# Optimization experiments

Measured on AMD Instinct MI355X. Metric: run time of the kernel, lower is better.

Reference implementation:

```python
import jax, jax.numpy as jnp
import numpy as np

N_NODES = 50000
IN_CH = 128
HID = 32
HEADS = 4
OUT_CH = 40
NEG_SLOPE = 0.2


def _glorot(key, shape):
    fan_in, fan_out = shape[-1], shape[0]
    lim = jnp.sqrt(6.0 / (fan_in + fan_out))
    return jax.random.uniform(key, shape, jnp.float32, -lim, lim)


def setup_inputs() -> dict:
    key = jax.random.key(0)
    ks = jax.random.split(key, 16)
    x = jax.random.normal(ks[0], (N_NODES, IN_CH), jnp.float32)
    edge_index = jax.random.randint(ks[1], (2, 800000), 0, N_NODES, jnp.int64)
    # layer 0: in -> hid, heads, concat
    W0 = _glorot(ks[2], (HEADS * HID, IN_CH))
    a_src0 = _glorot(ks[3], (HEADS, HID))
    a_dst0 = _glorot(ks[4], (HEADS, HID))
    b0 = jnp.zeros((HEADS * HID,), jnp.float32)
    # layer 1: hid*heads -> hid, heads, concat
    W1 = _glorot(ks[5], (HEADS * HID, HEADS * HID))
    a_src1 = _glorot(ks[6], (HEADS, HID))
    a_dst1 = _glorot(ks[7], (HEADS, HID))
    b1 = jnp.zeros((HEADS * HID,), jnp.float32)
    # layer 2: hid*heads -> out, 1 head, no concat (mean)
    W2 = _glorot(ks[8], (OUT_CH, HEADS * HID))
    a_src2 = _glorot(ks[9], (1, OUT_CH))
    a_dst2 = _glorot(ks[10], (1, OUT_CH))
    b2 = jnp.zeros((OUT_CH,), jnp.float32)
    return dict(x=x, edge_index=edge_index, W0=W0, a_src0=a_src0, a_dst0=a_dst0, b0=b0,
                W1=W1, a_src1=a_src1, a_dst1=a_dst1, b1=b1,
                W2=W2, a_src2=a_src2, a_dst2=a_dst2, b2=b2)


def _gat_conv(x, src, dst, W, a_src, a_dst, b, concat):
    # PyG GATConv (eval mode, dropout off, negative_slope=0.2)
    N = x.shape[0]
    H, C = a_src.shape
    h = (x @ W.T).reshape(N, H, C)                      # [N,H,C]
    al_s = jnp.sum(h * a_src, axis=-1)                  # [N,H]
    al_d = jnp.sum(h * a_dst, axis=-1)                  # [N,H]
    e = jax.nn.leaky_relu(al_s[src] + al_d[dst], NEG_SLOPE)  # [E,H]
    # segment softmax over destination nodes
    m = jax.ops.segment_max(e, dst, num_segments=N)     # [N,H]
    ex = jnp.exp(e - m[dst])
    den = jax.ops.segment_sum(ex, dst, num_segments=N)  # [N,H]
    alpha = ex / den[dst]                               # [E,H]
    out = jax.ops.segment_sum(h[src] * alpha[:, :, None], dst, num_segments=N)  # [N,H,C]
    out = out.reshape(N, H * C) if concat else out.mean(axis=1)
    return out + b


def reference(x, edge_index, W0, a_src0, a_dst0, b0, W1, a_src1, a_dst1, b1, W2, a_src2, a_dst2, b2):
    N = x.shape[0]
    loops = jnp.arange(N, dtype=edge_index.dtype)
    ei = jnp.concatenate([edge_index, jnp.stack([loops, loops])], axis=1)  # add self loops (PyG default)
    src, dst = ei[0], ei[1]
    h = _gat_conv(x, src, dst, W0, a_src0, a_dst0, b0, concat=True)
    h = jax.nn.elu(h)
    h = _gat_conv(h, src, dst, W1, a_src1, a_dst1, b1, concat=True)
    h = jax.nn.elu(h)
    h = _gat_conv(h, src, dst, W2, a_src2, a_dst2, b2, concat=False)
    return jax.nn.log_softmax(h, axis=1)
```

## Files before the change

### kernel.cpp

```cpp
#include <hip/hip_runtime.h>
#include <hip/hip_fp16.h>
#include <math.h>

typedef _Float16 f16x8 __attribute__((ext_vector_type(8)));
typedef _Float16 f16x4 __attribute__((ext_vector_type(4)));
typedef float f32x4 __attribute__((ext_vector_type(4)));

__device__ __forceinline__ int f2oi(float f) {
    int i = __float_as_int(f);
    return i >= 0 ? i : (i ^ 0x7FFFFFFF);
}
__device__ __forceinline__ float oi2f(int i) {
    return __int_as_float(i >= 0 ? i : (i ^ 0x7FFFFFFF));
}

template<int MT, int H>
__global__ __launch_bounds__(256) void gemm_mfma(const float* __restrict__ X,
                                                 const float* __restrict__ W,
                                                 const float* __restrict__ a_src,
                                                 const float* __restrict__ a_dst,
                                                 __half* __restrict__ Hout, int Mout,
                                                 float* __restrict__ als,
                                                 float* __restrict__ ald,
                                                 int* __restrict__ mint, int N) {
    constexpr int LDSB = (MT * 4096 > 16384) ? MT * 4096 : 16384;
    constexpr int HST = (MT == 8) ? 256 : 128;
    __shared__ char ldsb[LDSB];
    __shared__ int lmax[8];

    int tid = threadIdx.x;
    if (tid < 8) lmax[tid] = (int)0x80000000;

    const int nf4 = 16 * MT * 32;
    for (int idx = tid; idx < nf4; idx += 256) {
        int r = idx >> 5, c = idx & 31;
        float4 w = (r < Mout) ? reinterpret_cast<const float4*>(W)[(size_t)r * 32 + c]
                              : make_float4(0.f, 0.f, 0.f, 0.f);
        f16x4 hv;
        hv[0] = (_Float16)w.x; hv[1] = (_Float16)w.y;
        hv[2] = (_Float16)w.z; hv[3] = (_Float16)w.w;
        int byte = r * 256 + ((c * 8) ^ ((r & 7) << 4));
        *reinterpret_cast<f16x4*>(&ldsb[byte]) = hv;
    }
    __syncthreads();

    int l = tid & 63, wv = tid >> 6;
    int lr = l & 15, lk = l >> 4;
    f32x4 acc[2][MT];
#pragma unroll
    for (int rt = 0; rt < 2; rt++)
#pragma unroll
        for (int c = 0; c < MT; c++) acc[rt][c] = (f32x4){0.f, 0.f, 0.f, 0.f};

    const float* xp[2];
#pragma unroll
    for (int rt = 0; rt < 2; rt++) {
        int rg = blockIdx.x * 128 + rt * 64 + wv * 16 + lr;
        if (rg >= N) rg = N - 1;
        xp[rt] = X + (size_t)rg * 128 + lk * 8;
    }

#pragma unroll
    for (int k0 = 0; k0 < 128; k0 += 32) {
        f16x8 a[2];
#pragma unroll
        for (int rt = 0; rt < 2; rt++) {
            float4 x0 = *reinterpret_cast<const float4*>(xp[rt] + k0);
            float4 x1 = *reinterpret_cast<const float4*>(xp[rt] + k0 + 4);
            a[rt][0] = (_Float16)x0.x; a[rt][1] = (_Float16)x0.y;
            a[rt][2] = (_Float16)x0.z; a[rt][3] = (_Float16)x0.w;
            a[rt][4] = (_Float16)x1.x; a[rt][5] = (_Float16)x1.y;
            a[rt][6] = (_Float16)x1.z; a[rt][7] = (_Float16)x1.w;
        }
#pragma unroll
        for (int c = 0; c < MT; c++) {
            int n = 16 * c + lr;
            int byte = n * 256 + (((k0 + lk * 8) * 2) ^ ((n & 7) << 4));
            f16x8 b = *reinterpret_cast<const f16x8*>(&ldsb[byte]);
            acc[0][c] = __builtin_amdgcn_mfma_f32_16x16x32_f16(a[0], b, acc[0][c], 0, 0, 0);
            acc[1][c] = __builtin_amdgcn_mfma_f32_16x16x32_f16(a[1], b, acc[1][c], 0, 0, 0);
        }
    }
    __syncthreads();

#pragma unroll
    for (int rt = 0; rt < 2; rt++)
#pragma unroll
        for (int c = 0; c < MT; c++)
#pragma unroll
            for (int r = 0; r < 4; r++) {
                int rowl = rt * 64 + wv * 16 + lk * 4 + r;
                int col = 16 * c + lr;
                int byte = rowl * HST + ((col * 2) ^ ((rowl & 7) << 4));
                *reinterpret_cast<__half*>(&ldsb[byte]) = __float2half(acc[rt][c][r]);
            }
    __syncthreads();

    int row = tid >> 1, seg = tid & 1;
    int rowg = blockIdx.x * 128 + row;
    if (rowg < N) {
        const int rowB = Mout * 2;
        int segstart = (MT == 8) ? seg * 128 : seg * 48;
        int nch = (MT == 8) ? 8 : (seg ? 2 : 3);
        float hs[H], hd[H];
#pragma unroll
        for (int h = 0; h < H; h++) { hs[h] = 0.f; hd[h] = 0.f; }
        for (int i = 0; i < nch; i++) {
            int cb = segstart + i * 16;
            f16x8 v = *reinterpret_cast<const f16x8*>(
                &ldsb[row * HST + (cb ^ ((row & 7) << 4))]);
            *reinterpret_cast<f16x8*>((char*)Hout + (size_t)rowg * rowB + cb) = v;
            int hh = (H == 1) ? 0 : (cb >> 6);
            int colb = cb >> 1;
            float ps = 0.f, pd = 0.f;
#pragma unroll
            for (int j = 0; j < 8; j++) {
                float f = (float)v[j];
                ps = fmaf(f, a_src[colb + j], ps);
                pd = fmaf(f, a_dst[colb + j], pd);
            }
            hs[hh] += ps; hd[hh] += pd;
        }
        if (H == 4) {
#pragma unroll
            for (int t = 0; t < 2; t++) {
                int hh = 2 * seg + t;
                als[rowg * 4 + hh] = hs[hh];
                ald[rowg * 4 + hh] = hd[hh];
                atomicMax(&lmax[hh], f2oi(hs[hh]));
                atomicMax(&lmax[4 + hh], f2oi(hd[hh]));
            }
        } else {
            float s = hs[0] + __shfl_xor(hs[0], 1, 64);
            float d = hd[0] + __shfl_xor(hd[0], 1, 64);
            if (seg == 0) {
                als[rowg] = s; ald[rowg] = d;
                atomicMax(&lmax[0], f2oi(s));
                atomicMax(&lmax[4], f2oi(d));
            }
        }
    }
    __syncthreads();
    if (tid < H) atomicMax(&mint[tid], lmax[tid]);
    if (tid >= 8 && tid < 8 + H) atomicMax(&mint[4 + tid - 8], lmax[4 + tid - 8]);
}

__global__ __launch_bounds__(256) void p1_hist(const int* __restrict__ src,
                                               const int* __restrict__ dst,
                                               int E_real, int E_tot, int NB, int NBLK,
                                               int EPB, int* __restrict__ cntmat) {
    __shared__ int hist[1024];
    for (int i = threadIdx.x; i < NB; i += 256) hist[i] = 0;
    __syncthreads();
    int e0 = blockIdx.x * EPB;
    int e1 = min(e0 + EPB, E_tot);
    for (int e = e0 + threadIdx.x; e < e1; e += 256) {
        int d = (e < E_real) ? dst[e] : e - E_real;
        atomicAdd(&hist[d >> 6], 1);
    }
    __syncthreads();
    for (int b = threadIdx.x; b < NB; b += 256)
        cntmat[b * NBLK + blockIdx.x] = hist[b];
}

__global__ __launch_bounds__(256) void p_scancols(int* __restrict__ cntmat,
                                                  int* __restrict__ colTot, int NBLK) {
    __shared__ int sh[256];
    int b = blockIdx.x;
    int t = threadIdx.x;
    if (t < NBLK) sh[t] = cntmat[b * NBLK + t];
    __syncthreads();
    if (t == 0) {
        int run = 0;
        for (int i = 0; i < NBLK; i++) { int v = sh[i]; sh[i] = run; run += v; }
        colTot[b] = run;
    }
    __syncthreads();
    if (t < NBLK) cntmat[b * NBLK + t] = sh[t];
}

__global__ __launch_bounds__(256) void p_scancoarse(const int* __restrict__ colTot,
                                                    int* __restrict__ coarseOff,
                                                    int* __restrict__ offsets,
                                                    int NB, int N, int E_tot) {
    __shared__ int sh[256];
    int t = threadIdx.x, base = t * 4;
    int v0 = 0, v1 = 0, v2 = 0, v3 = 0;
    if (base + 0 < NB) v0 = colTot[base + 0];
    if (base + 1 < NB) v1 = colTot[base + 1];
    if (base + 2 < NB) v2 = colTot[base + 2];
    if (base + 3 < NB) v3 = colTot[base + 3];
    int s = v0 + v1 + v2 + v3;
    sh[t] = s;
    __syncthreads();
    for (int off = 1; off < 256; off <<= 1) {
        int u = (t >= off) ? sh[t - off] : 0;
        __syncthreads();
        sh[t] += u;
        __syncthreads();
    }
    int run = sh[t] - s;
    if (base + 0 < NB) { coarseOff[base + 0] = run; run += v0; }
    if (base + 1 < NB) { coarseOff[base + 1] = run; run += v1; }
    if (base + 2 < NB) { coarseOff[base + 2] = run; run += v2; }
    if (base + 3 < NB) { coarseOff[base + 3] = run; }
    if (t == 255) { coarseOff[NB] = sh[255]; offsets[N] = E_tot; }
}

__global__ __launch_bounds__(256) void p2_scatter(const int* __restrict__ src,
                                                  const int* __restrict__ dst,
                                                  int E_real, int E_tot, int NB, int NBLK,
                                                  int EPB, const int* __restrict__ cntmat,
                                                  const int* __restrict__ coarseOff,
                                                  int2* __restrict__ pairs) {
    __shared__ int cur[1024];
    for (int b = threadIdx.x; b < NB; b += 256)
        cur[b] = coarseOff[b] + cntmat[b * NBLK + blockIdx.x];
    __syncthreads();
    int e0 = blockIdx.x * EPB;
    int e1 = min(e0 + EPB, E_tot);
    for (int e = e0 + threadIdx.x; e < e1; e += 256) {
        int s, d;
        if (e < E_real) { s = src[e]; d = dst[e]; } else { s = d = e - E_real; }
        int pos = atomicAdd(&cur[d >> 6], 1);
        pairs[pos] = make_int2(s, d);
    }
}

__global__ __launch_bounds__(256) void p3_bucket(const int2* __restrict__ pairs,
                                                 const int* __restrict__ coarseOff,
                                                 int NB, int N, int* __restrict__ offsets,
                                                 int* __restrict__ csr_src) {
    __shared__ int lh[64], lc[64];
    int b = blockIdx.x;
    int beg = coarseOff[b], end = coarseOff[b + 1];
    int t = threadIdx.x;
    if (t < 64) lh[t] = 0;
    __syncthreads();
    for (int i = beg + t; i < end; i += 256)
        atomicAdd(&lh[pairs[i].y & 63], 1);
    __syncthreads();
    if (t < 64) {
        int v = lh[t];
        int run = v;
#pragma unroll
        for (int off = 1; off < 64; off <<= 1) {
            int o = __shfl_up(run, off, 64);
            if (t >= off) run += o;
        }
        int ex = run - v;
        lc[t] = ex;
        int node = b * 64 + t;
        if (node < N) offsets[node] = beg + ex;
    }
    __syncthreads();
    for (int i = beg + t; i < end; i += 256) {
        int2 p = pairs[i];
        int pos = atomicAdd(&lc[p.y & 63], 1);
        csr_src[beg + pos] = p.x;
    }
}

__global__ __launch_bounds__(256) void gat_agg128(const int* __restrict__ offsets,
                                                  const int* __restrict__ csr_src,
                                                  const __half* __restrict__ h,
                                                  const float* __restrict__ als,
                                                  const float* __restrict__ ald,
                                                  const int* __restrict__ mint,
                                                  const float* __restrict__ bias,
                                                  float* __restrict__ out, int N) {
    __shared__ float wlds[4][64][4];
    __shared__ int   slds[4][64];
    int wid = threadIdx.x >> 6;
    int lane = threadIdx.x & 63;
    int gwid = (blockIdx.x * 256 + threadIdx.x) >> 6;
    int nWaves = (gridDim.x * 256) >> 6;
    int hh = lane >> 4;
    const __half2* h2 = (const __half2*)h;
    const float4* als4 = (const float4*)als;
    const float4* ald4 = (const float4*)ald;
    float2 bv = ((const float2*)bias)[lane];

    float4 shift;
    {
        float v;
        v = oi2f(mint[0]) + oi2f(mint[4]); shift.x = v > 0.f ? v : 0.2f * v;
        v = oi2f(mint[1]) + oi2f(mint[5]); shift.y = v > 0.f ? v : 0.2f * v;
        v = oi2f(mint[2]) + oi2f(mint[6]); shift.z = v > 0.f ? v : 0.2f * v;
        v = oi2f(mint[3]) + oi2f(mint[7]); shift.w = v > 0.f ? v : 0.2f * v;
    }

    for (int n = gwid; n < N; n += nWaves) {
        int beg = offsets[n], end = offsets[n + 1];
        float4 adn = ald4[n];
        float accx = 0.f, accy = 0.f, den = 0.f;

        for (int c0 = beg; c0 < end; c0 += 64) {
            int e = c0 + lane;
            if (e < end) {
                int s = csr_src[e];
                float4 a4 = als4[s];
                float4 w; float v;
                v = a4.x + adn.x; v = v > 0.f ? v : 0.2f * v; w.x = __expf(v - shift.x);
                v = a4.y + adn.y; v = v > 0.f ? v : 0.2f * v; w.y = __expf(v - shift.y);
                v = a4.z + adn.z; v = v > 0.f ? v : 0.2f * v; w.z = __expf(v - shift.z);
                v = a4.w + adn.w; v = v > 0.f ? v : 0.2f * v; w.w = __expf(v - shift.w);
                *reinterpret_cast<float4*>(&wlds[wid][lane][0]) = w;
                slds[wid][lane] = s;
            }
            int cnt = end - c0; if (cnt > 64) cnt = 64;
            int p = 0;
            for (; p + 4 <= cnt; p += 4) {
                float w0 = wlds[wid][p][hh];     int s0 = slds[wid][p];
                float w1 = wlds[wid][p + 1][hh]; int s1 = slds[wid][p + 1];
                float w2 = wlds[wid][p + 2][hh]; int s2 = slds[wid][p + 2];
                float w3 = wlds[wid][p + 3][hh]; int s3 = slds[wid][p + 3];
                float2 f0 = __half22float2(h2[(size_t)s0 * 64 + lane]);
                float2 f1 = __half22float2(h2[(size_t)s1 * 64 + lane]);
                float2 f2 = __half22float2(h2[(size_t)s2 * 64 + lane]);
                float2 f3 = __half22float2(h2[(size_t)s3 * 64 + lane]);
                den += (w0 + w1) + (w2 + w3);
                accx = fmaf(f0.x, w0, fmaf(f1.x, w1, fmaf(f2.x, w2, fmaf(f3.x, w3, accx))));
                accy = fmaf(f0.y, w0, fmaf(f1.y, w1, fmaf(f2.y, w2, fmaf(f3.y, w3, accy))));
            }
            for (; p < cnt; ++p) {
                float w0 = wlds[wid][p][hh]; int s0 = slds[wid][p];
                float2 f0 = __half22float2(h2[(size_t)s0 * 64 + lane]);
                den += w0;
                accx = fmaf(f0.x, w0, accx);
                accy = fmaf(f0.y, w0, accy);
            }
        }
        float inv = 1.f / den;
        float r0 = accx * inv + bv.x;
        float r1 = accy * inv + bv.y;
        float2 o;
        o.x = r0 > 0.f ? r0 : expm1f(r0);
        o.y = r1 > 0.f ? r1 : expm1f(r1);
        ((float2*)out)[(size_t)n * 64 + lane] = o;
    }
}

__global__ __launch_bounds__(256) void gat_agg40_lsm(const int* __restrict__ offsets,
                                                     const int* __restrict__ csr_src,
                                                     const __half* __restrict__ h,
                                                     const float* __restrict__ als,
                                                     const float* __restrict__ ald,
                                                     const int* __restrict__ mint,
                                                     const float* __restrict__ b2,
                                                     float* __restrict__ out, int N) {
    __shared__ float wlds[4][64];
    __shared__ int   slds[4][64];
    int wid = threadIdx.x >> 6;
    int lane = threadIdx.x & 63;
    int gwid = (blockIdx.x * 256 + threadIdx.x) >> 6;
    int nWaves = (gridDim.x * 256) >> 6;

    float shift;
    {
        float v = oi2f(mint[0]) + oi2f(mint[4]);
        shift = v > 0.f ? v : 0.2f * v;
    }

    for (int n = gwid; n < N; n += nWaves) {
        int beg = offsets[n], end = offsets[n + 1];
        float adn = ald[n];
        float acc = 0.f, den = 0.f;

        for (int c0 = beg; c0 < end; c0 += 64) {
            int e = c0 + lane;
            if (e < end) {
                int s = csr_src[e];
                float v = als[s] + adn; v = v > 0.f ? v : 0.2f * v;
                wlds[wid][lane] = __expf(v - shift);
                slds[wid][lane] = s;
            }
            int cnt = end - c0; if (cnt > 64) cnt = 64;
            int p = 0;
            for (; p + 4 <= cnt; p += 4) {
                float w0 = wlds[wid][p];     int s0 = slds[wid][p];
                float w1 = wlds[wid][p + 1]; int s1 = slds[wid][p + 1];
                float w2 = wlds[wid][p + 2]; int s2 = slds[wid][p + 2];
                float w3 = wlds[wid][p + 3]; int s3 = slds[wid][p + 3];
                float h0 = (lane < 40) ? __half2float(h[(size_t)s0 * 40 + lane]) : 0.f;
                float h1 = (lane < 40) ? __half2float(h[(size_t)s1 * 40 + lane]) : 0.f;
                float h2v = (lane < 40) ? __half2float(h[(size_t)s2 * 40 + lane]) : 0.f;
                float h3 = (lane < 40) ? __half2float(h[(size_t)s3 * 40 + lane]) : 0.f;
                den += (w0 + w1) + (w2 + w3);
                acc = fmaf(h0, w0, fmaf(h1, w1, fmaf(h2v, w2, fmaf(h3, w3, acc))));
            }
            for (; p < cnt; ++p) {
                float w0 = wlds[wid][p]; int s0 = slds[wid][p];
                float h0 = (lane < 40) ? __half2float(h[(size_t)s0 * 40 + lane]) : 0.f;
                den += w0;
                acc = fmaf(h0, w0, acc);
            }
        }
        float val = (lane < 40) ? acc / den + b2[lane] : -INFINITY;
        float mx = val;
#pragma unroll
        for (int off = 32; off >= 1; off >>= 1) mx = fmaxf(mx, __shfl_xor(mx, off, 64));
        float pe = (lane < 40) ? __expf(val - mx) : 0.f;
        float sum = pe;
#pragma unroll
        for (int off = 32; off >= 1; off >>= 1) sum += __shfl_xor(sum, off, 64);
        if (lane < 40) out[n * 40 + lane] = val - mx - logf(sum);
    }
}

extern "C" void kernel_launch(void* const* d_in, const int* in_sizes, int n_in,
                              void* d_out, int out_size, void* d_ws, size_t ws_size,
                              hipStream_t stream) {
    const float* x      = (const float*)d_in[0];
    const int*   ei     = (const int*)d_in[1];
    const float* W0     = (const float*)d_in[2];
    const float* a_src0 = (const float*)d_in[3];
    const float* a_dst0 = (const float*)d_in[4];
    const float* b0     = (const float*)d_in[5];
    const float* W1     = (const float*)d_in[6];
    const float* a_src1 = (const float*)d_in[7];
    const float* a_dst1 = (const float*)d_in[8];
    const float* b1     = (const float*)d_in[9];
    const float* W2     = (const float*)d_in[10];
    const float* a_src2 = (const float*)d_in[11];
    const float* a_dst2 = (const float*)d_in[12];
    const float* b2     = (const float*)d_in[13];

    const int N = in_sizes[0] / 128;
    const int E_real = in_sizes[1] / 2;
    const int E_tot = E_real + N;
    const int* src = ei;
    const int* dst = ei + E_real;

    const int EPB  = 4096;
    const int NBLK = (E_tot + EPB - 1) / EPB;
    const int NB   = (N + 63) >> 6;

    unsigned char* ws = (unsigned char*)d_ws;
    const size_t szH16 = (size_t)N * 128 * sizeof(__half);
    const size_t szAcc = (size_t)N * 128 * sizeof(float);
    size_t off = 0;
    __half* bufH    = (__half*)(ws + off); off += szH16;
    float*  bufAcc  = (float*)(ws + off);  off += szAcc;
    int2*   pairs   = (int2*)(ws + off);   off += (size_t)E_tot * sizeof(int2);
    int*    csr_src = (int*)(ws + off);    off += (size_t)E_tot * sizeof(int);
    float*  als     = (float*)(ws + off);  off += (size_t)N * 4 * sizeof(float);
    float*  ald     = (float*)(ws + off);  off += (size_t)N * 4 * sizeof(float);
    int*    cntmat  = (int*)(ws + off);    off += (size_t)NB * NBLK * sizeof(int);
    int*    colTot  = (int*)(ws + off);    off += (size_t)NB * sizeof(int);
    int*    coarseOff = (int*)(ws + off);  off += (size_t)(NB + 1) * sizeof(int);
    int*    offsets = (int*)(ws + off);    off += (size_t)(N + 1) * sizeof(int);
    int*    mint    = (int*)(ws + off);    off += 24 * sizeof(int);

    const int B = 256;
    const int gRows128 = (N + 127) / 128;
    const int gAgg  = 2048;

    hipMemsetAsync(mint, 0x80, 24 * sizeof(int), stream);
    p1_hist<<<NBLK, B, 0, stream>>>(src, dst, E_real, E_tot, NB, NBLK, EPB, cntmat);
    p_scancols<<<NB, B, 0, stream>>>(cntmat, colTot, NBLK);
    p_scancoarse<<<1, B, 0, stream>>>(colTot, coarseOff, offsets, NB, N, E_tot);
    p2_scatter<<<NBLK, B, 0, stream>>>(src, dst, E_real, E_tot, NB, NBLK, EPB, cntmat, coarseOff, pairs);
    p3_bucket<<<NB, B, 0, stream>>>(pairs, coarseOff, NB, N, offsets, csr_src);

    gemm_mfma<8, 4><<<gRows128, B, 0, stream>>>(x, W0, a_src0, a_dst0, bufH, 128, als, ald, mint, N);
    gat_agg128<<<gAgg, B, 0, stream>>>(offsets, csr_src, bufH, als, ald, mint, b0, bufAcc, N);

    gemm_mfma<8, 4><<<gRows128, B, 0, stream>>>(bufAcc, W1, a_src1, a_dst1, bufH, 128, als, ald, mint + 8, N);
    gat_agg128<<<gAgg, B, 0, stream>>>(offsets, csr_src, bufH, als, ald, mint + 8, b1, bufAcc, N);

    gemm_mfma<3, 1><<<gRows128, B, 0, stream>>>(bufAcc, W2, a_src2, a_dst2, bufH, 40, als, ald, mint + 16, N);
    gat_agg40_lsm<<<gAgg, B, 0, stream>>>(offsets, csr_src, bufH, als, ald, mint + 16, b2,
                                          (float*)d_out, N);
}
```

Before: 238.1 us.

## Split edge attention weights into separate precompute kernels before aggregation

Moves the per-edge leaky-relu/exp attention weight computation out of the aggregation kernels into dedicated edge_w4/edge_w1 kernels that write weights to a workspace buffer aliased with the pairs array. The aggregation kernels then read weights and sources directly from global memory in 8-wide unrolled batches, with no LDS staging or wave-level chunking. This is meant to remove LDS round trips and improve memory-level parallelism in the gather loop. In exchange it adds three launches and an extra write and read of the per-edge weight array (16 bytes per edge for the four-head layers).

```diff
diff --git a/kernel.cpp b/kernel.cpp
--- a/kernel.cpp
+++ b/kernel.cpp
@@ -261,26 +261,17 @@
     }
 }
 
-__global__ __launch_bounds__(256) void gat_agg128(const int* __restrict__ offsets,
-                                                  const int* __restrict__ csr_src,
-                                                  const __half* __restrict__ h,
-                                                  const float* __restrict__ als,
-                                                  const float* __restrict__ ald,
-                                                  const int* __restrict__ mint,
-                                                  const float* __restrict__ bias,
-                                                  float* __restrict__ out, int N) {
-    __shared__ float wlds[4][64][4];
-    __shared__ int   slds[4][64];
-    int wid = threadIdx.x >> 6;
+__global__ __launch_bounds__(256) void edge_w4(const int* __restrict__ offsets,
+                                               const int* __restrict__ csr_src,
+                                               const float* __restrict__ als,
+                                               const float* __restrict__ ald,
+                                               const int* __restrict__ mint,
+                                               float4* __restrict__ wexp, int N) {
     int lane = threadIdx.x & 63;
     int gwid = (blockIdx.x * 256 + threadIdx.x) >> 6;
     int nWaves = (gridDim.x * 256) >> 6;
-    int hh = lane >> 4;
-    const __half2* h2 = (const __half2*)h;
     const float4* als4 = (const float4*)als;
     const float4* ald4 = (const float4*)ald;
-    float2 bv = ((const float2*)bias)[lane];
-
     float4 shift;
     {
         float v;
@@ -289,47 +280,86 @@
         v = oi2f(mint[2]) + oi2f(mint[6]); shift.z = v > 0.f ? v : 0.2f * v;
         v = oi2f(mint[3]) + oi2f(mint[7]); shift.w = v > 0.f ? v : 0.2f * v;
     }
-
     for (int n = gwid; n < N; n += nWaves) {
         int beg = offsets[n], end = offsets[n + 1];
         float4 adn = ald4[n];
+        for (int e = beg + lane; e < end; e += 64) {
+            int s = csr_src[e];
+            float4 a4 = als4[s];
+            float4 w; float v;
+            v = a4.x + adn.x; v = v > 0.f ? v : 0.2f * v; w.x = __expf(v - shift.x);
+            v = a4.y + adn.y; v = v > 0.f ? v : 0.2f * v; w.y = __expf(v - shift.y);
+            v = a4.z + adn.z; v = v > 0.f ? v : 0.2f * v; w.z = __expf(v - shift.z);
+            v = a4.w + adn.w; v = v > 0.f ? v : 0.2f * v; w.w = __expf(v - shift.w);
+            wexp[e] = w;
+        }
+    }
+}
+
+__global__ __launch_bounds__(256) void edge_w1(const int* __restrict__ offsets,
+                                               const int* __restrict__ csr_src,
+                                               const float* __restrict__ als,
+                                               const float* __restrict__ ald,
+                                               const int* __restrict__ mint,
+                                               float* __restrict__ wexp, int N) {
+    int lane = threadIdx.x & 63;
+    int gwid = (blockIdx.x * 256 + threadIdx.x) >> 6;
+    int nWaves = (gridDim.x * 256) >> 6;
+    float shift;
+    {
+        float v = oi2f(mint[0]) + oi2f(mint[4]);
+        shift = v > 0.f ? v : 0.2f * v;
+    }
+    for (int n = gwid; n < N; n += nWaves) {
+        int beg = offsets[n], end = offsets[n + 1];
+        float adn = ald[n];
+        for (int e = beg + lane; e < end; e += 64) {
+            int s = csr_src[e];
+            float v = als[s] + adn; v = v > 0.f ? v : 0.2f * v;
+            wexp[e] = __expf(v - shift);
+        }
+    }
+}
+
+__global__ __launch_bounds__(256) void gat_agg128(const int* __restrict__ offsets,
+                                                  const int* __restrict__ csr_src,
+                                                  const __half* __restrict__ h,
+                                                  const float* __restrict__ wexp,
+                                                  const float* __restrict__ bias,
+                                                  float* __restrict__ out, int N) {
+    int lane = threadIdx.x & 63;
+    int gwid = (blockIdx.x * 256 + threadIdx.x) >> 6;
+    int nWaves = (gridDim.x * 256) >> 6;
+    int hh = lane >> 4;
+    const __half2* h2 = (const __half2*)h;
+    float2 bv = ((const float2*)bias)[lane];
+
+    for (int n = gwid; n < N; n += nWaves) {
+        int beg = offsets[n], end = offsets[n + 1];
         float accx = 0.f, accy = 0.f, den = 0.f;
-
-        for (int c0 = beg; c0 < end; c0 += 64) {
-            int e = c0 + lane;
-            if (e < end) {
-                int s = csr_src[e];
-                float4 a4 = als4[s];
-                float4 w; float v;
-                v = a4.x + adn.x; v = v > 0.f ? v : 0.2f * v; w.x = __expf(v - shift.x);
-                v = a4.y + adn.y; v = v > 0.f ? v : 0.2f * v; w.y = __expf(v - shift.y);
-                v = a4.z + adn.z; v = v > 0.f ? v : 0.2f * v; w.z = __expf(v - shift.z);
-                v = a4.w + adn.w; v = v > 0.f ? v : 0.2f * v; w.w = __expf(v - shift.w);
-                *reinterpret_cast<float4*>(&wlds[wid][lane][0]) = w;
-                slds[wid][lane] = s;
-            }
-            int cnt = end - c0; if (cnt > 64) cnt = 64;
-            int p = 0;
-            for (; p + 4 <= cnt; p += 4) {
-                float w0 = wlds[wid][p][hh];     int s0 = slds[wid][p];
-                float w1 = wlds[wid][p + 1][hh]; int s1 = slds[wid][p + 1];
-                float w2 = wlds[wid][p + 2][hh]; int s2 = slds[wid][p + 2];
-                float w3 = wlds[wid][p + 3][hh]; int s3 = slds[wid][p + 3];
-                float2 f0 = __half22float2(h2[(size_t)s0 * 64 + lane]);
-                float2 f1 = __half22float2(h2[(size_t)s1 * 64 + lane]);
-                float2 f2 = __half22float2(h2[(size_t)s2 * 64 + lane]);
-                float2 f3 = __half22float2(h2[(size_t)s3 * 64 + lane]);
-                den += (w0 + w1) + (w2 + w3);
-                accx = fmaf(f0.x, w0, fmaf(f1.x, w1, fmaf(f2.x, w2, fmaf(f3.x, w3, accx))));
-                accy = fmaf(f0.y, w0, fmaf(f1.y, w1, fmaf(f2.y, w2, fmaf(f3.y, w3, accy))));
-            }
-            for (; p < cnt; ++p) {
-                float w0 = wlds[wid][p][hh]; int s0 = slds[wid][p];
-                float2 f0 = __half22float2(h2[(size_t)s0 * 64 + lane]);
-                den += w0;
-                accx = fmaf(f0.x, w0, accx);
-                accy = fmaf(f0.y, w0, accy);
-            }
+        int p = beg;
+        for (; p + 8 <= end; p += 8) {
+            float w[8]; int s[8];
+#pragma unroll
+            for (int j = 0; j < 8; j++) {
+                w[j] = wexp[(size_t)(p + j) * 4 + hh];
+                s[j] = csr_src[p + j];
+            }
+#pragma unroll
+            for (int j = 0; j < 8; j++) {
+                float2 f = __half22float2(h2[(size_t)s[j] * 64 + lane]);
+                den += w[j];
+                accx = fmaf(f.x, w[j], accx);
+                accy = fmaf(f.y, w[j], accy);
+            }
+        }
+        for (; p < end; ++p) {
+            float w0 = wexp[(size_t)p * 4 + hh];
+            int s0 = csr_src[p];
+            float2 f = __half22float2(h2[(size_t)s0 * 64 + lane]);
+            den += w0;
+            accx = fmaf(f.x, w0, accx);
+            accy = fmaf(f.y, w0, accy);
         }
         float inv = 1.f / den;
         float r0 = accx * inv + bv.x;
@@ -344,57 +374,37 @@
 __global__ __launch_bounds__(256) void gat_agg40_lsm(const int* __restrict__ offsets,
                                                      const int* __restrict__ csr_src,
                                                      const __half* __restrict__ h,
-                                                     const float* __restrict__ als,
-                                                     const float* __restrict__ ald,
-                                                     const int* __restrict__ mint,
+                                                     const float* __restrict__ wexp,
                                                      const float* __restrict__ b2,
                                                      float* __restrict__ out, int N) {
-    __shared__ float wlds[4][64];
-    __shared__ int   slds[4][64];
-    int wid = threadIdx.x >> 6;
     int lane = threadIdx.x & 63;
     int gwid = (blockIdx.x * 256 + threadIdx.x) >> 6;
     int nWaves = (gridDim.x * 256) >> 6;
 
-    float shift;
-    {
-        float v = oi2f(mint[0]) + oi2f(mint[4]);
-        shift = v > 0.f ? v : 0.2f * v;
-    }
-
     for (int n = gwid; n < N; n += nWaves) {
         int beg = offsets[n], end = offsets[n + 1];
-        float adn = ald[n];
         float acc = 0.f, den = 0.f;
-
-        for (int c0 = beg; c0 < end; c0 += 64) {
-            int e = c0 + lane;
-            if (e < end) {
-                int s = csr_src[e];
-                float v = als[s] + adn; v = v > 0.f ? v : 0.2f * v;
-                wlds[wid][lane] = __expf(v - shift);
-                slds[wid][lane] = s;
-            }
-            int cnt = end - c0; if (cnt > 64) cnt = 64;
-            int p = 0;
-            for (; p + 4 <= cnt; p += 4) {
-                float w0 = wlds[wid][p];     int s0 = slds[wid][p];
-                float w1 = wlds[wid][p + 1]; int s1 = slds[wid][p + 1];
-                float w2 = wlds[wid][p + 2]; int s2 = slds[wid][p + 2];
-                float w3 = wlds[wid][p + 3]; int s3 = slds[wid][p + 3];
-                float h0 = (lane < 40) ? __half2float(h[(size_t)s0 * 40 + lane]) : 0.f;
-                float h1 = (lane < 40) ? __half2float(h[(size_t)s1 * 40 + lane]) : 0.f;
-                float h2v = (lane < 40) ? __half2float(h[(size_t)s2 * 40 + lane]) : 0.f;
-                float h3 = (lane < 40) ? __half2float(h[(size_t)s3 * 40 + lane]) : 0.f;
-                den += (w0 + w1) + (w2 + w3);
-                acc = fmaf(h0, w0, fmaf(h1, w1, fmaf(h2v, w2, fmaf(h3, w3, acc))));
-            }
-            for (; p < cnt; ++p) {
-                float w0 = wlds[wid][p]; int s0 = slds[wid][p];
-                float h0 = (lane < 40) ? __half2float(h[(size_t)s0 * 40 + lane]) : 0.f;
-                den += w0;
-                acc = fmaf(h0, w0, acc);
-            }
+        int p = beg;
+        for (; p + 8 <= end; p += 8) {
+            float w[8]; int s[8];
+#pragma unroll
+            for (int j = 0; j < 8; j++) {
+                w[j] = wexp[p + j];
+                s[j] = csr_src[p + j];
+            }
+#pragma unroll
+            for (int j = 0; j < 8; j++) {
+                float hv = (lane < 40) ? __half2float(h[(size_t)s[j] * 40 + lane]) : 0.f;
+                den += w[j];
+                acc = fmaf(hv, w[j], acc);
+            }
+        }
+        for (; p < end; ++p) {
+            float w0 = wexp[p];
+            int s0 = csr_src[p];
+            float hv = (lane < 40) ? __half2float(h[(size_t)s0 * 40 + lane]) : 0.f;
+            den += w0;
+            acc = fmaf(hv, w0, acc);
         }
         float val = (lane < 40) ? acc / den + b2[lane] : -INFINITY;
         float mx = val;
@@ -437,20 +447,20 @@
     const int NB   = (N + 63) >> 6;
 
     unsigned char* ws = (unsigned char*)d_ws;
-    const size_t szH16 = (size_t)N * 128 * sizeof(__half);
-    const size_t szAcc = (size_t)N * 128 * sizeof(float);
     size_t off = 0;
-    __half* bufH    = (__half*)(ws + off); off += szH16;
-    float*  bufAcc  = (float*)(ws + off);  off += szAcc;
-    int2*   pairs   = (int2*)(ws + off);   off += (size_t)E_tot * sizeof(int2);
+    __half* bufH    = (__half*)(ws + off); off += (size_t)N * 128 * sizeof(__half);
+    float*  bufAcc  = (float*)(ws + off);  off += (size_t)N * 128 * sizeof(float);
     int*    csr_src = (int*)(ws + off);    off += (size_t)E_tot * sizeof(int);
     float*  als     = (float*)(ws + off);  off += (size_t)N * 4 * sizeof(float);
     float*  ald     = (float*)(ws + off);  off += (size_t)N * 4 * sizeof(float);
-    int*    cntmat  = (int*)(ws + off);    off += (size_t)NB * NBLK * sizeof(int);
+    int*    offsets = (int*)(ws + off);    off += (size_t)(N + 1) * sizeof(int);
     int*    colTot  = (int*)(ws + off);    off += (size_t)NB * sizeof(int);
     int*    coarseOff = (int*)(ws + off);  off += (size_t)(NB + 1) * sizeof(int);
-    int*    offsets = (int*)(ws + off);    off += (size_t)(N + 1) * sizeof(int);
     int*    mint    = (int*)(ws + off);    off += 24 * sizeof(int);
+    int*    cntmat  = (int*)(ws + off);    off += (size_t)NB * NBLK * sizeof(int);
+    off = (off + 15) & ~(size_t)15;
+    int2*   pairs   = (int2*)(ws + off);
+    float*  wexp    = (float*)(ws + off);  off += (size_t)E_tot * 4 * sizeof(float);
 
     const int B = 256;
     const int gRows128 = (N + 127) / 128;
@@ -464,12 +474,15 @@
     p3_bucket<<<NB, B, 0, stream>>>(pairs, coarseOff, NB, N, offsets, csr_src);
 
     gemm_mfma<8, 4><<<gRows128, B, 0, stream>>>(x, W0, a_src0, a_dst0, bufH, 128, als, ald, mint, N);
-    gat_agg128<<<gAgg, B, 0, stream>>>(offsets, csr_src, bufH, als, ald, mint, b0, bufAcc, N);
+    edge_w4<<<gAgg, B, 0, stream>>>(offsets, csr_src, als, ald, mint, (float4*)wexp, N);
+    gat_agg128<<<gAgg, B, 0, stream>>>(offsets, csr_src, bufH, wexp, b0, bufAcc, N);
 
     gemm_mfma<8, 4><<<gRows128, B, 0, stream>>>(bufAcc, W1, a_src1, a_dst1, bufH, 128, als, ald, mint + 8, N);
-    gat_agg128<<<gAgg, B, 0, stream>>>(offsets, csr_src, bufH, als, ald, mint + 8, b1, bufAcc, N);
+    edge_w4<<<gAgg, B, 0, stream>>>(offsets, csr_src, als, ald, mint + 8, (float4*)wexp, N);
+    gat_agg128<<<gAgg, B, 0, stream>>>(offsets, csr_src, bufH, wexp, b1, bufAcc, N);
 
     gemm_mfma<3, 1><<<gRows128, B, 0, stream>>>(bufAcc, W2, a_src2, a_dst2, bufH, 40, als, ald, mint + 16, N);
-    gat_agg40_lsm<<<gAgg, B, 0, stream>>>(offsets, csr_src, bufH, als, ald, mint + 16, b2,
+    edge_w1<<<gAgg, B, 0, stream>>>(offsets, csr_src, als, ald, mint + 16, wexp, N);
+    gat_agg40_lsm<<<gAgg, B, 0, stream>>>(offsets, csr_src, bufH, wexp, b2,
                                           (float*)d_out, N);
 }
```

Result: slower. 280.2 us (+17.7%).

## Vectorize neighbor gathers across edge groups and pack CSR build pairs

Applied to the files above, without the earlier changes.

The aggregation kernels now split each wave into four 16-lane groups that process four edges at once, each lane loading 8 (or 4) halves with one wide load, then combine group partials with cross-lane shuffles. This targets per-edge gather latency and raises memory-level parallelism. The CSR build packs (src,dst) into one 32-bit int instead of int2, halving scatter traffic. The packing relies on node indices fitting in 16 bits, and the shuffle reduction adds a little work per node.

```diff
diff --git a/kernel.cpp b/kernel.cpp
--- a/kernel.cpp
+++ b/kernel.cpp
@@ -212,7 +212,7 @@
                                                   int E_real, int E_tot, int NB, int NBLK,
                                                   int EPB, const int* __restrict__ cntmat,
                                                   const int* __restrict__ coarseOff,
-                                                  int2* __restrict__ pairs) {
+                                                  int* __restrict__ pairs) {
     __shared__ int cur[1024];
     for (int b = threadIdx.x; b < NB; b += 256)
         cur[b] = coarseOff[b] + cntmat[b * NBLK + blockIdx.x];
@@ -223,11 +223,11 @@
         int s, d;
         if (e < E_real) { s = src[e]; d = dst[e]; } else { s = d = e - E_real; }
         int pos = atomicAdd(&cur[d >> 6], 1);
-        pairs[pos] = make_int2(s, d);
-    }
-}
-
-__global__ __launch_bounds__(256) void p3_bucket(const int2* __restrict__ pairs,
+        pairs[pos] = (s << 16) | d;
+    }
+}
+
+__global__ __launch_bounds__(256) void p3_bucket(const int* __restrict__ pairs,
                                                  const int* __restrict__ coarseOff,
                                                  int NB, int N, int* __restrict__ offsets,
                                                  int* __restrict__ csr_src) {
@@ -238,7 +238,7 @@
     if (t < 64) lh[t] = 0;
     __syncthreads();
     for (int i = beg + t; i < end; i += 256)
-        atomicAdd(&lh[pairs[i].y & 63], 1);
+        atomicAdd(&lh[pairs[i] & 63], 1);
     __syncthreads();
     if (t < 64) {
         int v = lh[t];
@@ -255,9 +255,9 @@
     }
     __syncthreads();
     for (int i = beg + t; i < end; i += 256) {
-        int2 p = pairs[i];
-        int pos = atomicAdd(&lc[p.y & 63], 1);
-        csr_src[beg + pos] = p.x;
+        int pk = pairs[i];
+        int pos = atomicAdd(&lc[pk & 63], 1);
+        csr_src[beg + pos] = ((unsigned)pk) >> 16;
     }
 }
 
@@ -273,27 +273,31 @@
     __shared__ int   slds[4][64];
     int wid = threadIdx.x >> 6;
     int lane = threadIdx.x & 63;
+    int g = lane >> 4, j = lane & 15, hd = j >> 2;
     int gwid = (blockIdx.x * 256 + threadIdx.x) >> 6;
     int nWaves = (gridDim.x * 256) >> 6;
-    int hh = lane >> 4;
-    const __half2* h2 = (const __half2*)h;
+    const f16x8* h8 = (const f16x8*)h;
     const float4* als4 = (const float4*)als;
     const float4* ald4 = (const float4*)ald;
-    float2 bv = ((const float2*)bias)[lane];
-
-    float4 shift;
+
+    float4 shiftv;
     {
         float v;
-        v = oi2f(mint[0]) + oi2f(mint[4]); shift.x = v > 0.f ? v : 0.2f * v;
-        v = oi2f(mint[1]) + oi2f(mint[5]); shift.y = v > 0.f ? v : 0.2f * v;
-        v = oi2f(mint[2]) + oi2f(mint[6]); shift.z = v > 0.f ? v : 0.2f * v;
-        v = oi2f(mint[3]) + oi2f(mint[7]); shift.w = v > 0.f ? v : 0.2f * v;
-    }
+        v = oi2f(mint[0]) + oi2f(mint[4]); shiftv.x = v > 0.f ? v : 0.2f * v;
+        v = oi2f(mint[1]) + oi2f(mint[5]); shiftv.y = v > 0.f ? v : 0.2f * v;
+        v = oi2f(mint[2]) + oi2f(mint[6]); shiftv.z = v > 0.f ? v : 0.2f * v;
+        v = oi2f(mint[3]) + oi2f(mint[7]); shiftv.w = v > 0.f ? v : 0.2f * v;
+    }
+    float4 bv0 = ((const float4*)bias)[j * 2];
+    float4 bv1 = ((const float4*)bias)[j * 2 + 1];
 
     for (int n = gwid; n < N; n += nWaves) {
         int beg = offsets[n], end = offsets[n + 1];
         float4 adn = ald4[n];
-        float accx = 0.f, accy = 0.f, den = 0.f;
+        float acc[8];
+#pragma unroll
+        for (int k = 0; k < 8; k++) acc[k] = 0.f;
+        float den = 0.f;
 
         for (int c0 = beg; c0 < end; c0 += 64) {
             int e = c0 + lane;
@@ -301,43 +305,48 @@
                 int s = csr_src[e];
                 float4 a4 = als4[s];
                 float4 w; float v;
-                v = a4.x + adn.x; v = v > 0.f ? v : 0.2f * v; w.x = __expf(v - shift.x);
-                v = a4.y + adn.y; v = v > 0.f ? v : 0.2f * v; w.y = __expf(v - shift.y);
-                v = a4.z + adn.z; v = v > 0.f ? v : 0.2f * v; w.z = __expf(v - shift.z);
-                v = a4.w + adn.w; v = v > 0.f ? v : 0.2f * v; w.w = __expf(v - shift.w);
+                v = a4.x + adn.x; v = v > 0.f ? v : 0.2f * v; w.x = __expf(v - shiftv.x);
+                v = a4.y + adn.y; v = v > 0.f ? v : 0.2f * v; w.y = __expf(v - shiftv.y);
+                v = a4.z + adn.z; v = v > 0.f ? v : 0.2f * v; w.z = __expf(v - shiftv.z);
+                v = a4.w + adn.w; v = v > 0.f ? v : 0.2f * v; w.w = __expf(v - shiftv.w);
                 *reinterpret_cast<float4*>(&wlds[wid][lane][0]) = w;
                 slds[wid][lane] = s;
             }
             int cnt = end - c0; if (cnt > 64) cnt = 64;
-            int p = 0;
-            for (; p + 4 <= cnt; p += 4) {
-                float w0 = wlds[wid][p][hh];     int s0 = slds[wid][p];
-                float w1 = wlds[wid][p + 1][hh]; int s1 = slds[wid][p + 1];
-                float w2 = wlds[wid][p + 2][hh]; int s2 = slds[wid][p + 2];
-                float w3 = wlds[wid][p + 3][hh]; int s3 = slds[wid][p + 3];
-                float2 f0 = __half22float2(h2[(size_t)s0 * 64 + lane]);
-                float2 f1 = __half22float2(h2[(size_t)s1 * 64 + lane]);
-                float2 f2 = __half22float2(h2[(size_t)s2 * 64 + lane]);
-                float2 f3 = __half22float2(h2[(size_t)s3 * 64 + lane]);
-                den += (w0 + w1) + (w2 + w3);
-                accx = fmaf(f0.x, w0, fmaf(f1.x, w1, fmaf(f2.x, w2, fmaf(f3.x, w3, accx))));
-                accy = fmaf(f0.y, w0, fmaf(f1.y, w1, fmaf(f2.y, w2, fmaf(f3.y, w3, accy))));
-            }
-            for (; p < cnt; ++p) {
-                float w0 = wlds[wid][p][hh]; int s0 = slds[wid][p];
-                float2 f0 = __half22float2(h2[(size_t)s0 * 64 + lane]);
-                den += w0;
-                accx = fmaf(f0.x, w0, accx);
-                accy = fmaf(f0.y, w0, accy);
-            }
-        }
-        float inv = 1.f / den;
-        float r0 = accx * inv + bv.x;
-        float r1 = accy * inv + bv.y;
-        float2 o;
-        o.x = r0 > 0.f ? r0 : expm1f(r0);
-        o.y = r1 > 0.f ? r1 : expm1f(r1);
-        ((float2*)out)[(size_t)n * 64 + lane] = o;
+            for (int p = 0; p < cnt; p += 4) {
+                int e2 = p + g;
+                int ec = (e2 < cnt) ? e2 : cnt - 1;
+                int s = slds[wid][ec];
+                float w = wlds[wid][ec][hd];
+                if (e2 >= cnt) w = 0.f;
+                f16x8 hv = h8[(size_t)s * 16 + j];
+                den += w;
+#pragma unroll
+                for (int k = 0; k < 8; k++)
+                    acc[k] = fmaf((float)hv[k], w, acc[k]);
+            }
+        }
+#pragma unroll
+        for (int off = 16; off <= 32; off <<= 1) {
+            den += __shfl_xor(den, off, 64);
+#pragma unroll
+            for (int k = 0; k < 8; k++) acc[k] += __shfl_xor(acc[k], off, 64);
+        }
+        if (g == 0) {
+            float inv = 1.f / den;
+            float4 o0, o1;
+            float r;
+            r = acc[0] * inv + bv0.x; o0.x = r > 0.f ? r : expm1f(r);
+            r = acc[1] * inv + bv0.y; o0.y = r > 0.f ? r : expm1f(r);
+            r = acc[2] * inv + bv0.z; o0.z = r > 0.f ? r : expm1f(r);
+            r = acc[3] * inv + bv0.w; o0.w = r > 0.f ? r : expm1f(r);
+            r = acc[4] * inv + bv1.x; o1.x = r > 0.f ? r : expm1f(r);
+            r = acc[5] * inv + bv1.y; o1.y = r > 0.f ? r : expm1f(r);
+            r = acc[6] * inv + bv1.z; o1.z = r > 0.f ? r : expm1f(r);
+            r = acc[7] * inv + bv1.w; o1.w = r > 0.f ? r : expm1f(r);
+            float4* op = (float4*)(out + (size_t)n * 128 + j * 8);
+            op[0] = o0; op[1] = o1;
+        }
     }
 }
 
@@ -353,6 +362,7 @@
     __shared__ int   slds[4][64];
     int wid = threadIdx.x >> 6;
     int lane = threadIdx.x & 63;
+    int g = lane >> 4, j = lane & 15;
     int gwid = (blockIdx.x * 256 + threadIdx.x) >> 6;
     int nWaves = (gridDim.x * 256) >> 6;
 
@@ -361,11 +371,15 @@
         float v = oi2f(mint[0]) + oi2f(mint[4]);
         shift = v > 0.f ? v : 0.2f * v;
     }
+    float4 bv = (j < 10) ? ((const float4*)b2)[j] : make_float4(0.f, 0.f, 0.f, 0.f);
 
     for (int n = gwid; n < N; n += nWaves) {
         int beg = offsets[n], end = offsets[n + 1];
         float adn = ald[n];
-        float acc = 0.f, den = 0.f;
+        float acc[4];
+#pragma unroll
+        for (int k = 0; k < 4; k++) acc[k] = 0.f;
+        float den = 0.f;
 
         for (int c0 = beg; c0 < end; c0 += 64) {
             int e = c0 + lane;
@@ -376,35 +390,52 @@
                 slds[wid][lane] = s;
             }
             int cnt = end - c0; if (cnt > 64) cnt = 64;
-            int p = 0;
-            for (; p + 4 <= cnt; p += 4) {
-                float w0 = wlds[wid][p];     int s0 = slds[wid][p];
-                float w1 = wlds[wid][p + 1]; int s1 = slds[wid][p + 1];
-                float w2 = wlds[wid][p + 2]; int s2 = slds[wid][p + 2];
-                float w3 = wlds[wid][p + 3]; int s3 = slds[wid][p + 3];
-                float h0 = (lane < 40) ? __half2float(h[(size_t)s0 * 40 + lane]) : 0.f;
-                float h1 = (lane < 40) ? __half2float(h[(size_t)s1 * 40 + lane]) : 0.f;
-                float h2v = (lane < 40) ? __half2float(h[(size_t)s2 * 40 + lane]) : 0.f;
-                float h3 = (lane < 40) ? __half2float(h[(size_t)s3 * 40 + lane]) : 0.f;
-                den += (w0 + w1) + (w2 + w3);
-                acc = fmaf(h0, w0, fmaf(h1, w1, fmaf(h2v, w2, fmaf(h3, w3, acc))));
-            }
-            for (; p < cnt; ++p) {
-                float w0 = wlds[wid][p]; int s0 = slds[wid][p];
-                float h0 = (lane < 40) ? __half2float(h[(size_t)s0 * 40 + lane]) : 0.f;
-                den += w0;
-                acc = fmaf(h0, w0, acc);
-            }
-        }
-        float val = (lane < 40) ? acc / den + b2[lane] : -INFINITY;
-        float mx = val;
-#pragma unroll
-        for (int off = 32; off >= 1; off >>= 1) mx = fmaxf(mx, __shfl_xor(mx, off, 64));
-        float pe = (lane < 40) ? __expf(val - mx) : 0.f;
-        float sum = pe;
-#pragma unroll
-        for (int off = 32; off >= 1; off >>= 1) sum += __shfl_xor(sum, off, 64);
-        if (lane < 40) out[n * 40 + lane] = val - mx - logf(sum);
+            for (int p = 0; p < cnt; p += 4) {
+                int e2 = p + g;
+                int ec = (e2 < cnt) ? e2 : cnt - 1;
+                int s = slds[wid][ec];
+                float w = wlds[wid][ec];
+                if (e2 >= cnt) w = 0.f;
+                den += w;
+                if (j < 10) {
+                    f16x4 hv = reinterpret_cast<const f16x4*>(h + (size_t)s * 40)[j];
+#pragma unroll
+                    for (int k = 0; k < 4; k++)
+                        acc[k] = fmaf((float)hv[k], w, acc[k]);
+                }
+            }
+        }
+#pragma unroll
+        for (int off = 16; off <= 32; off <<= 1) {
+            den += __shfl_xor(den, off, 64);
+#pragma unroll
+            for (int k = 0; k < 4; k++) acc[k] += __shfl_xor(acc[k], off, 64);
+        }
+        float inv = 1.f / den;
+        float val[4];
+        float m = -INFINITY;
+#pragma unroll
+        for (int k = 0; k < 4; k++) {
+            val[k] = (j < 10) ? acc[k] * inv + ((const float*)&bv)[k] : -INFINITY;
+            m = fmaxf(m, val[k]);
+        }
+#pragma unroll
+        for (int off = 8; off >= 1; off >>= 1) m = fmaxf(m, __shfl_xor(m, off, 64));
+        float pe = 0.f;
+#pragma unroll
+        for (int k = 0; k < 4; k++)
+            if (j < 10) pe += __expf(val[k] - m);
+#pragma unroll
+        for (int off = 8; off >= 1; off >>= 1) pe += __shfl_xor(pe, off, 64);
+        if (g == 0 && j < 10) {
+            float lsum = logf(pe);
+            float4 o;
+            o.x = val[0] - m - lsum;
+            o.y = val[1] - m - lsum;
+            o.z = val[2] - m - lsum;
+            o.w = val[3] - m - lsum;
+            ((float4*)(out + (size_t)n * 40))[j] = o;
+        }
     }
 }
 
@@ -437,20 +468,18 @@
     const int NB   = (N + 63) >> 6;
 
     unsigned char* ws = (unsigned char*)d_ws;
-    const size_t szH16 = (size_t)N * 128 * sizeof(__half);
-    const size_t szAcc = (size_t)N * 128 * sizeof(float);
     size_t off = 0;
-    __half* bufH    = (__half*)(ws + off); off += szH16;
-    float*  bufAcc  = (float*)(ws + off);  off += szAcc;
-    int2*   pairs   = (int2*)(ws + off);   off += (size_t)E_tot * sizeof(int2);
+    __half* bufH    = (__half*)(ws + off); off += (size_t)N * 128 * sizeof(__half);
+    float*  bufAcc  = (float*)(ws + off);  off += (size_t)N * 128 * sizeof(float);
     int*    csr_src = (int*)(ws + off);    off += (size_t)E_tot * sizeof(int);
+    int*    pairs   = (int*)(ws + off);    off += (size_t)E_tot * sizeof(int);
     float*  als     = (float*)(ws + off);  off += (size_t)N * 4 * sizeof(float);
     float*  ald     = (float*)(ws + off);  off += (size_t)N * 4 * sizeof(float);
-    int*    cntmat  = (int*)(ws + off);    off += (size_t)NB * NBLK * sizeof(int);
+    int*    offsets = (int*)(ws + off);    off += (size_t)(N + 1) * sizeof(int);
     int*    colTot  = (int*)(ws + off);    off += (size_t)NB * sizeof(int);
     int*    coarseOff = (int*)(ws + off);  off += (size_t)(NB + 1) * sizeof(int);
-    int*    offsets = (int*)(ws + off);    off += (size_t)(N + 1) * sizeof(int);
     int*    mint    = (int*)(ws + off);    off += 24 * sizeof(int);
+    int*    cntmat  = (int*)(ws + off);    off += (size_t)NB * NBLK * sizeof(int);
 
     const int B = 256;
     const int gRows128 = (N + 127) / 128;
```

New measurement: 222.4 us. 1.07x faster.
